# Kernel tuning notes

Hardware: AMD Instinct MI355X
Metric: run time of the kernel (lower is better)

The kernel has to match this reference:

```python
import jax, jax.numpy as jnp
import numpy as np

B, S, H = 4, 4096, 256

def setup_inputs() -> dict:
    key = jax.random.key(0)
    ks = jax.random.split(key, 7)
    s = 1.0 / np.sqrt(H)
    return {
        "x": jax.random.normal(ks[0], (B, S, H), dtype=jnp.float32),
        "Wq": jax.random.normal(ks[1], (H, H), dtype=jnp.float32) * s,
        "bq": jax.random.normal(ks[2], (H,), dtype=jnp.float32) * 0.01,
        "Wk": jax.random.normal(ks[3], (H, H), dtype=jnp.float32) * s,
        "bk": jax.random.normal(ks[4], (H,), dtype=jnp.float32) * 0.01,
        "Wv": jax.random.normal(ks[5], (H, H), dtype=jnp.float32) * s,
        "bv": jax.random.normal(ks[6], (H,), dtype=jnp.float32) * 0.01,
    }

def reference(x, Wq, bq, Wk, bk, Wv, bv):
    # Linear projections (torch Linear: x @ W^T + b; here W stored as [in,out])
    Q = jnp.einsum('bsh,hd->bsd', x, Wq) + bq
    K = jnp.einsum('bsh,hd->bsd', x, Wk) + bk
    V = jnp.einsum('bsh,hd->bsd', x, Wv) + bv
    scale = 1.0 / jnp.sqrt(jnp.float32(x.shape[-1]))
    scores = jnp.einsum('bqd,bkd->bqk', Q, K) * scale  # [B,S,S]
    weights = jax.nn.softmax(scores, axis=-1)
    return jnp.einsum('bqk,bkd->bqd', weights, V)
```

## Files before the change

### kernel.cpp

```cpp
#include <hip/hip_runtime.h>
#include <hip/hip_bf16.h>
#include <stdint.h>
#include <stddef.h>


typedef __bf16 bf16;
typedef _Float16 f16;
typedef __attribute__((ext_vector_type(4))) __bf16 bf16x4;
typedef __attribute__((ext_vector_type(8))) __bf16 bf16x8;
typedef __attribute__((ext_vector_type(4))) float f32x4;
typedef __attribute__((ext_vector_type(4))) _Float16 f16x4;
typedef __attribute__((ext_vector_type(8))) _Float16 f16x8;

#define S_LEN 4096
#define HDIM  256
#define PSTRIDE ((size_t)16384 * 256)

__device__ __forceinline__ f32x4 mfma16(bf16x8 a, bf16x8 b, f32x4 c) {
  return __builtin_amdgcn_mfma_f32_16x16x32_bf16(a, b, c, 0, 0, 0);
}

__device__ __forceinline__ void gld_lds16(const void* g, void* l) {
  __builtin_amdgcn_global_load_lds(
      (const __attribute__((address_space(1))) void*)g,
      (__attribute__((address_space(3))) void*)l, 16, 0, 0);
}

__device__ __forceinline__ float fast_exp2(float x) {
  float r;
  asm("v_exp_f32 %0, %1" : "=v"(r) : "v"(x));
  return r;
}

#define BAR_VMCNT4() do { \
  asm volatile("s_waitcnt vmcnt(4)" ::: "memory"); \
  __builtin_amdgcn_s_barrier(); \
  asm volatile("" ::: "memory"); \
  __builtin_amdgcn_sched_barrier(0); } while (0)
#define BAR_VMCNT0() do { \
  asm volatile("s_waitcnt vmcnt(0)" ::: "memory"); \
  __builtin_amdgcn_s_barrier(); \
  asm volatile("" ::: "memory"); \
  __builtin_amdgcn_sched_barrier(0); } while (0)

__global__ __launch_bounds__(256) void wt_kernel(
    const float* __restrict__ Wq, const float* __restrict__ Wk,
    const float* __restrict__ Wv, bf16* __restrict__ WT) {
  __shared__ float tile[32][33];
  int bid = blockIdx.x;
  int m = bid >> 6;
  int t = bid & 63;
  int hb = (t >> 3) * 32;
  int db = (t & 7) * 32;
  const float* W = (m == 0) ? Wq : (m == 1) ? Wk : Wv;
  bf16* o = WT + m * 65536;
  int ty = threadIdx.x >> 3;
  int tx = threadIdx.x & 7;
  float4 v = *(const float4*)(W + (size_t)(hb + ty) * 256 + db + tx * 4);
  tile[ty][tx * 4 + 0] = v.x; tile[ty][tx * 4 + 1] = v.y;
  tile[ty][tx * 4 + 2] = v.z; tile[ty][tx * 4 + 3] = v.w;
  __syncthreads();
  bf16x4 h = {(bf16)tile[tx * 4 + 0][ty], (bf16)tile[tx * 4 + 1][ty],
              (bf16)tile[tx * 4 + 2][ty], (bf16)tile[tx * 4 + 3][ty]};
  *(bf16x4*)(o + (size_t)(db + ty) * 256 + hb + tx * 4) = h;
}

__global__ __launch_bounds__(256, 3) void proj_kernel(
    const float* __restrict__ x, const bf16* __restrict__ WT,
    const float* __restrict__ bq, const float* __restrict__ bk,
    const float* __restrict__ bv,
    bf16* __restrict__ Qb, char* __restrict__ KV) {
  __shared__ __align__(16) char smem[34816];
  int tid = threadIdx.x;
  int row0 = blockIdx.x * 64;
  int m = blockIdx.y;

#pragma unroll
  for (int i = 0; i < 16; ++i) {
    int c = i * 256 + tid;
    int r = c >> 6, c4 = c & 63;
    float4 v = *(const float4*)(x + (size_t)(row0 + r) * 256 + c4 * 4);
    bf16x4 b4 = {(bf16)v.x, (bf16)v.y, (bf16)v.z, (bf16)v.w};
    *(bf16x4*)(smem + r * 512 + ((c4 * 8) ^ ((r & 7) << 4))) = b4;
  }
  __syncthreads();

  int w = tid >> 6, lane = tid & 63, lg = lane >> 4, l15 = lane & 15;
  int ar = w * 16 + l15;
  int swz = (l15 & 7) << 4;
  bf16x8 af[8];
#pragma unroll
  for (int ks = 0; ks < 8; ++ks)
    af[ks] = *(const bf16x8*)(smem + ar * 512 + ((ks * 64 + lg * 16) ^ swz));
  __syncthreads();

  int b = row0 >> 12, t0 = (row0 & 4095) >> 5;
  const bf16* Wm = WT + m * 65536;
  const float* bias = (m == 0) ? bq : (m == 1) ? bk : bv;

#pragma unroll
  for (int i = 0; i < 4; ++i) {
    int c = w * 4 + i;
    gld_lds16(Wm + (c * 16 + l15) * 256 + lg * 8, smem + c * 1024 + lane * 16);
  }
  __syncthreads();

  f32x4 acc[16];
#pragma unroll
  for (int dt = 0; dt < 16; ++dt) acc[dt] = f32x4{0.f, 0.f, 0.f, 0.f};

  for (int ks = 0; ks < 8; ++ks) {
    const char* wb = smem + (ks & 1) * 16384;
    if (ks + 1 < 8) {
      char* wn = smem + ((ks + 1) & 1) * 16384;
#pragma unroll
      for (int i = 0; i < 4; ++i) {
        int c = w * 4 + i;
        gld_lds16(Wm + (c * 16 + l15) * 256 + (ks + 1) * 32 + lg * 8,
                  wn + c * 1024 + lane * 16);
      }
    }
    __builtin_amdgcn_s_setprio(1);
#pragma unroll
    for (int dt = 0; dt < 16; ++dt) {
      bf16x8 wf = *(const bf16x8*)(wb + dt * 1024 + lane * 16);
      acc[dt] = mfma16(af[ks], wf, acc[dt]);
    }
    __builtin_amdgcn_s_setprio(0);
    __syncthreads();
  }

  if (m == 0) {
#pragma unroll
    for (int dt = 0; dt < 16; ++dt) {
      float bb = bias[dt * 16 + l15];
#pragma unroll
      for (int rr = 0; rr < 4; ++rr) {
        int srow = row0 + w * 16 + 4 * lg + rr;
        Qb[(size_t)srow * 256 + dt * 16 + l15] = (bf16)(acc[dt][rr] + bb);
      }
    }
  } else if (m == 1) {
    bf16* sm16 = (bf16*)smem;
#pragma unroll
    for (int dt = 0; dt < 16; ++dt) {
      float bb = bias[dt * 16 + l15];
#pragma unroll
      for (int rr = 0; rr < 4; ++rr) {
        int sl = w * 16 + 4 * lg + rr;
        sm16[sl * 264 + dt * 16 + l15] = (bf16)(acc[dt][rr] + bb);
      }
    }
    __syncthreads();
    int tt = tid >> 7, c = (tid >> 3) & 15, j0 = (tid & 7) * 8;
    char* dst = KV + ((size_t)(b * 128 + t0 + tt)) * 32768 + c * 1024 + j0 * 16;
#pragma unroll
    for (int u = 0; u < 8; ++u) {
      int l = j0 + u;
      bf16x8 v8 = *(const bf16x8*)(sm16 + (tt * 32 + (c & 1) * 16 + (l & 15)) * 264
                                   + (c >> 1) * 32 + (l >> 4) * 8);
      *(bf16x8*)(dst + u * 16) = v8;
    }
  } else {
    bf16* smV = (bf16*)smem;
#pragma unroll
    for (int dt = 0; dt < 16; ++dt) {
      float bb = bias[dt * 16 + l15];
      bf16x4 h = {(bf16)(acc[dt][0] + bb), (bf16)(acc[dt][1] + bb),
                  (bf16)(acc[dt][2] + bb), (bf16)(acc[dt][3] + bb)};
      *(bf16x4*)(smV + (dt * 16 + l15) * 68 + w * 16 + 4 * lg) = h;
    }
    __syncthreads();
    int tt = tid >> 7, c = (tid >> 3) & 15, j0 = (tid & 7) * 8;
    char* dst = KV + ((size_t)(b * 128 + t0 + tt)) * 32768 + 16384
                + c * 1024 + j0 * 16;
#pragma unroll
    for (int u = 0; u < 8; ++u) {
      int l = j0 + u;
      const bf16* p = smV + (c * 16 + (l & 15)) * 68 + tt * 32 + 4 * (l >> 4);
      bf16x4 lo = *(const bf16x4*)p;
      bf16x4 hi = *(const bf16x4*)(p + 16);
      bf16x8 v8 = __builtin_shufflevector(lo, hi, 0, 1, 2, 3, 4, 5, 6, 7);
      *(bf16x8*)(dst + u * 16) = v8;
    }
  }
}

__global__ __launch_bounds__(256, 2) void attn_kernel(
    const bf16* __restrict__ Qb, const char* __restrict__ KV,
    f16* __restrict__ P, float* __restrict__ ml, int nsplit, int ntiles) {
  __shared__ __align__(16) char smem[65536];

  int id = blockIdx.x;
  int b, sp, qb;
  if (nsplit == 4)      { int g = id & 15; b = g & 3;  sp = g >> 2; qb = id >> 4; }
  else if (nsplit == 2) { int g = id & 7;  b = g >> 1; sp = g & 1;  qb = id >> 3; }
  else                  { b = id & 3; sp = 0; qb = id >> 2; }

  int tid = threadIdx.x;
  int w = tid >> 6, lane = tid & 63, lg = lane >> 4, l15 = lane & 15;

  const char* kvsrc = KV + ((size_t)(b * 128 + sp * ntiles)) * 32768;

  int qrow0 = b * S_LEN + qb * 128 + w * 32 + l15;
  bf16x8 qf[2][8];
#pragma unroll
  for (int qs = 0; qs < 2; ++qs) {
    const bf16* Qr = Qb + (size_t)(qrow0 + qs * 16) * HDIM;
#pragma unroll
    for (int ks = 0; ks < 8; ++ks)
      qf[qs][ks] = *(const bf16x8*)(Qr + ks * 32 + lg * 8);
  }

  f32x4 acc[2][16];
#pragma unroll
  for (int qs = 0; qs < 2; ++qs)
#pragma unroll
    for (int dt = 0; dt < 16; ++dt) acc[qs][dt] = f32x4{0.f, 0.f, 0.f, 0.f};
  float lsum[2] = {0.f, 0.f};
  const float C = 0.09016844005556021f;

#pragma unroll
  for (int i = 0; i < 8; ++i)
    gld_lds16(kvsrc + i * 4096 + tid * 16, smem + i * 4096 + tid * 16);
  BAR_VMCNT0();

  for (int t = 0; t < ntiles; ++t) {
    int cur = (t & 1) << 15;
    const char* kb = smem + cur;
    const char* vb = kb + 16384;
    const char* s2 = kvsrc + (size_t)(t + 1) * 32768;
    char* d2 = smem + (cur ^ 32768);
    bool pre = (t + 1 < ntiles);

    if (pre) {
#pragma unroll
      for (int i = 0; i < 4; ++i)
        gld_lds16(s2 + i * 4096 + tid * 16, d2 + i * 4096 + tid * 16);
    }

    f32x4 st[2][2];
    st[0][0] = f32x4{0.f, 0.f, 0.f, 0.f}; st[0][1] = st[0][0];
    st[1][0] = st[0][0];                   st[1][1] = st[0][0];
    __builtin_amdgcn_s_setprio(1);
#pragma unroll
    for (int ks = 0; ks < 8; ++ks) {
      bf16x8 k0 = *(const bf16x8*)(kb + (ks * 2 + 0) * 1024 + lane * 16);
      bf16x8 k1 = *(const bf16x8*)(kb + (ks * 2 + 1) * 1024 + lane * 16);
      st[0][0] = mfma16(k0, qf[0][ks], st[0][0]);
      st[1][0] = mfma16(k0, qf[1][ks], st[1][0]);
      st[0][1] = mfma16(k1, qf[0][ks], st[0][1]);
      st[1][1] = mfma16(k1, qf[1][ks], st[1][1]);
    }
    __builtin_amdgcn_s_setprio(0);

    if (pre) BAR_VMCNT4(); else BAR_VMCNT0();

    if (pre) {
#pragma unroll
      for (int i = 4; i < 8; ++i)
        gld_lds16(s2 + i * 4096 + tid * 16, d2 + i * 4096 + tid * 16);
    }

    bf16x8 pf[2];
#pragma unroll
    for (int qs = 0; qs < 2; ++qs) {
      float ps = 0.f;
#pragma unroll
      for (int e = 0; e < 8; ++e) {
        float pv = fast_exp2(st[qs][e >> 2][e & 3] * C);
        ps += pv;
        pf[qs][e] = (bf16)pv;
      }
      lsum[qs] += ps;
    }

    __builtin_amdgcn_s_setprio(1);
#pragma unroll
    for (int dt = 0; dt < 16; ++dt) {
      bf16x8 vf = *(const bf16x8*)(vb + dt * 1024 + lane * 16);
      acc[0][dt] = mfma16(vf, pf[0], acc[0][dt]);
      acc[1][dt] = mfma16(vf, pf[1], acc[1][dt]);
    }
    __builtin_amdgcn_s_setprio(0);

    if (pre) BAR_VMCNT4();
  }

  f16* Pp = P + (size_t)sp * PSTRIDE;
#pragma unroll
  for (int qs = 0; qs < 2; ++qs) {
    float l = lsum[qs];
    l += __shfl_xor(l, 16, 64);
    l += __shfl_xor(l, 32, 64);
    int qrow = qrow0 + qs * 16;
    f16* prow = Pp + (size_t)qrow * HDIM;
#pragma unroll
    for (int dt = 0; dt < 16; ++dt) {
      f32x4 a = acc[qs][dt];
      f16x4 h = {(f16)a[0], (f16)a[1], (f16)a[2], (f16)a[3]};
      *(f16x4*)(prow + dt * 16 + 4 * lg) = h;
    }
    if (lane < 16) ml[sp * 16384 + qrow] = l;
  }
}

__global__ __launch_bounds__(256) void combine_kernel(
    float* __restrict__ out, const f16* __restrict__ P,
    const float* __restrict__ ml, int nsplit) {
  int chunk = blockIdx.x * 256 + threadIdx.x;
  int q = chunk >> 5;
  size_t base = (size_t)chunk * 8;

  float l = 0.f;
  float o[8] = {0.f, 0.f, 0.f, 0.f, 0.f, 0.f, 0.f, 0.f};
  for (int sp = 0; sp < nsplit; ++sp) {
    l += ml[sp * 16384 + q];
    f16x8 v = *(const f16x8*)(P + sp * PSTRIDE + base);
#pragma unroll
    for (int j = 0; j < 8; ++j) o[j] += (float)v[j];
  }
  float inv = 1.0f / l;
  f32x4 o0 = {o[0] * inv, o[1] * inv, o[2] * inv, o[3] * inv};
  f32x4 o1 = {o[4] * inv, o[5] * inv, o[6] * inv, o[7] * inv};
  *(f32x4*)(out + base) = o0;
  *(f32x4*)(out + base + 4) = o1;
}

extern "C" void kernel_launch(void* const* d_in, const int* in_sizes, int n_in,
                              void* d_out, int out_size, void* d_ws, size_t ws_size,
                              hipStream_t stream) {
  (void)in_sizes; (void)n_in; (void)out_size;
  const float* x  = (const float*)d_in[0];
  const float* Wq = (const float*)d_in[1];
  const float* bq = (const float*)d_in[2];
  const float* Wk = (const float*)d_in[3];
  const float* bk = (const float*)d_in[4];
  const float* Wv = (const float*)d_in[5];
  const float* bv = (const float*)d_in[6];

  char* ws = (char*)d_ws;
  bf16*  Qb = (bf16*)(ws);
  char*  KV = ws + (8u << 20);
  bf16*  WT = (bf16*)(ws + (24u << 20));
  float* ml = (float*)(ws + (24u << 20) + (512u << 10));
  f16*   P  = (f16*)(ws + (26u << 20));

  size_t need4 = ((size_t)26 << 20) + 4 * ((size_t)8 << 20);
  size_t need2 = ((size_t)26 << 20) + 2 * ((size_t)8 << 20);
  int nsplit = (ws_size >= need4) ? 4 : (ws_size >= need2) ? 2 : 1;
  int ntiles = (S_LEN / nsplit) / 32;
  int nblocks = 128 * nsplit;

  wt_kernel<<<192, 256, 0, stream>>>(Wq, Wk, Wv, WT);
  proj_kernel<<<dim3(256, 3), 256, 0, stream>>>(x, WT, bq, bk, bv, Qb, KV);
  attn_kernel<<<nblocks, 256, 0, stream>>>(Qb, KV, P, ml, nsplit, ntiles);
  combine_kernel<<<2048, 256, 0, stream>>>((float*)d_out, P, ml, nsplit);
}
```

Before: 109.5 us.

## Switch attention MFMAs from 16x16x32 to 32x32x16 with matching K/V layout

Replaces the 16x16x32 bf16 MFMA tiling in the attention kernel with 32x32x16 MFMAs. Each wave now owns 32 query rows as one tile, so QK^T takes 16 larger MFMAs per tile and PV takes 16 instead of 32 smaller ones. The projection kernel's K and V repacking into global memory is changed to match the 32-row operand layout. The goal is fewer MFMA issues and fewer LDS fragment reads per FLOP, at the cost of different register pressure and a different output write pattern.

```diff
diff --git a/kernel.cpp b/kernel.cpp
--- a/kernel.cpp
+++ b/kernel.cpp
@@ -9,6 +9,7 @@
 typedef __attribute__((ext_vector_type(4))) __bf16 bf16x4;
 typedef __attribute__((ext_vector_type(8))) __bf16 bf16x8;
 typedef __attribute__((ext_vector_type(4))) float f32x4;
+typedef __attribute__((ext_vector_type(16))) float f32x16;
 typedef __attribute__((ext_vector_type(4))) _Float16 f16x4;
 typedef __attribute__((ext_vector_type(8))) _Float16 f16x8;
 
@@ -18,6 +19,9 @@
 
 __device__ __forceinline__ f32x4 mfma16(bf16x8 a, bf16x8 b, f32x4 c) {
   return __builtin_amdgcn_mfma_f32_16x16x32_bf16(a, b, c, 0, 0, 0);
+}
+__device__ __forceinline__ f32x16 mfma32(bf16x8 a, bf16x8 b, f32x16 c) {
+  return __builtin_amdgcn_mfma_f32_32x32x16_bf16(a, b, c, 0, 0, 0);
 }
 
 __device__ __forceinline__ void gld_lds16(const void* g, void* l) {
@@ -157,8 +161,8 @@
 #pragma unroll
     for (int u = 0; u < 8; ++u) {
       int l = j0 + u;
-      bf16x8 v8 = *(const bf16x8*)(sm16 + (tt * 32 + (c & 1) * 16 + (l & 15)) * 264
-                                   + (c >> 1) * 32 + (l >> 4) * 8);
+      bf16x8 v8 = *(const bf16x8*)(sm16 + (tt * 32 + (l & 31)) * 264
+                                   + c * 16 + (l >> 5) * 8);
       *(bf16x8*)(dst + u * 16) = v8;
     }
   } else {
@@ -171,16 +175,18 @@
       *(bf16x4*)(smV + (dt * 16 + l15) * 68 + w * 16 + 4 * lg) = h;
     }
     __syncthreads();
-    int tt = tid >> 7, c = (tid >> 3) & 15, j0 = (tid & 7) * 8;
+    int tt = tid >> 7, c2 = (tid >> 3) & 15, j0 = (tid & 7) * 8;
+    int dt = c2 >> 1, ks = c2 & 1;
     char* dst = KV + ((size_t)(b * 128 + t0 + tt)) * 32768 + 16384
-                + c * 1024 + j0 * 16;
+                + c2 * 1024 + j0 * 16;
 #pragma unroll
     for (int u = 0; u < 8; ++u) {
       int l = j0 + u;
-      const bf16* p = smV + (c * 16 + (l & 15)) * 68 + tt * 32 + 4 * (l >> 4);
+      const bf16* p = smV + (dt * 32 + (l & 31)) * 68 + tt * 32
+                      + ks * 16 + 4 * (l >> 5);
       bf16x4 lo = *(const bf16x4*)p;
-      bf16x4 hi = *(const bf16x4*)(p + 16);
-      bf16x8 v8 = __builtin_shufflevector(lo, hi, 0, 1, 2, 3, 4, 5, 6, 7);
+      bf16x4 hi4 = *(const bf16x4*)(p + 8);
+      bf16x8 v8 = __builtin_shufflevector(lo, hi4, 0, 1, 2, 3, 4, 5, 6, 7);
       *(bf16x8*)(dst + u * 16) = v8;
     }
   }
@@ -198,26 +204,23 @@
   else                  { b = id & 3; sp = 0; qb = id >> 2; }
 
   int tid = threadIdx.x;
-  int w = tid >> 6, lane = tid & 63, lg = lane >> 4, l15 = lane & 15;
+  int w = tid >> 6, lane = tid & 63, hi = lane >> 5, l31 = lane & 31;
 
   const char* kvsrc = KV + ((size_t)(b * 128 + sp * ntiles)) * 32768;
 
-  int qrow0 = b * S_LEN + qb * 128 + w * 32 + l15;
-  bf16x8 qf[2][8];
-#pragma unroll
-  for (int qs = 0; qs < 2; ++qs) {
-    const bf16* Qr = Qb + (size_t)(qrow0 + qs * 16) * HDIM;
-#pragma unroll
-    for (int ks = 0; ks < 8; ++ks)
-      qf[qs][ks] = *(const bf16x8*)(Qr + ks * 32 + lg * 8);
-  }
-
-  f32x4 acc[2][16];
-#pragma unroll
-  for (int qs = 0; qs < 2; ++qs)
-#pragma unroll
-    for (int dt = 0; dt < 16; ++dt) acc[qs][dt] = f32x4{0.f, 0.f, 0.f, 0.f};
-  float lsum[2] = {0.f, 0.f};
+  int qrow = b * S_LEN + qb * 128 + w * 32 + l31;
+  const bf16* Qr = Qb + (size_t)qrow * HDIM;
+  bf16x8 qf[16];
+#pragma unroll
+  for (int c = 0; c < 16; ++c)
+    qf[c] = *(const bf16x8*)(Qr + c * 16 + hi * 8);
+
+  f32x16 acc[8];
+#pragma unroll
+  for (int dt = 0; dt < 8; ++dt)
+#pragma unroll
+    for (int r = 0; r < 16; ++r) acc[dt][r] = 0.f;
+  float lsum = 0.f;
   const float C = 0.09016844005556021f;
 
 #pragma unroll
@@ -239,18 +242,14 @@
         gld_lds16(s2 + i * 4096 + tid * 16, d2 + i * 4096 + tid * 16);
     }
 
-    f32x4 st[2][2];
-    st[0][0] = f32x4{0.f, 0.f, 0.f, 0.f}; st[0][1] = st[0][0];
-    st[1][0] = st[0][0];                   st[1][1] = st[0][0];
+    f32x16 st;
+#pragma unroll
+    for (int r = 0; r < 16; ++r) st[r] = 0.f;
     __builtin_amdgcn_s_setprio(1);
 #pragma unroll
-    for (int ks = 0; ks < 8; ++ks) {
-      bf16x8 k0 = *(const bf16x8*)(kb + (ks * 2 + 0) * 1024 + lane * 16);
-      bf16x8 k1 = *(const bf16x8*)(kb + (ks * 2 + 1) * 1024 + lane * 16);
-      st[0][0] = mfma16(k0, qf[0][ks], st[0][0]);
-      st[1][0] = mfma16(k0, qf[1][ks], st[1][0]);
-      st[0][1] = mfma16(k1, qf[0][ks], st[0][1]);
-      st[1][1] = mfma16(k1, qf[1][ks], st[1][1]);
+    for (int c = 0; c < 16; ++c) {
+      bf16x8 kf = *(const bf16x8*)(kb + c * 1024 + lane * 16);
+      st = mfma32(kf, qf[c], st);
     }
     __builtin_amdgcn_s_setprio(0);
 
@@ -262,47 +261,44 @@
         gld_lds16(s2 + i * 4096 + tid * 16, d2 + i * 4096 + tid * 16);
     }
 
+    float p[16];
+    float ps = 0.f;
+#pragma unroll
+    for (int r = 0; r < 16; ++r) {
+      p[r] = fast_exp2(st[r] * C);
+      ps += p[r];
+    }
+    lsum += ps;
     bf16x8 pf[2];
 #pragma unroll
-    for (int qs = 0; qs < 2; ++qs) {
-      float ps = 0.f;
-#pragma unroll
-      for (int e = 0; e < 8; ++e) {
-        float pv = fast_exp2(st[qs][e >> 2][e & 3] * C);
-        ps += pv;
-        pf[qs][e] = (bf16)pv;
+    for (int ks = 0; ks < 2; ++ks)
+#pragma unroll
+      for (int e = 0; e < 8; ++e) pf[ks][e] = (bf16)p[e + 8 * ks];
+
+    __builtin_amdgcn_s_setprio(1);
+#pragma unroll
+    for (int ks = 0; ks < 2; ++ks)
+#pragma unroll
+      for (int dt = 0; dt < 8; ++dt) {
+        bf16x8 vf = *(const bf16x8*)(vb + (dt * 2 + ks) * 1024 + lane * 16);
+        acc[dt] = mfma32(vf, pf[ks], acc[dt]);
       }
-      lsum[qs] += ps;
-    }
-
-    __builtin_amdgcn_s_setprio(1);
-#pragma unroll
-    for (int dt = 0; dt < 16; ++dt) {
-      bf16x8 vf = *(const bf16x8*)(vb + dt * 1024 + lane * 16);
-      acc[0][dt] = mfma16(vf, pf[0], acc[0][dt]);
-      acc[1][dt] = mfma16(vf, pf[1], acc[1][dt]);
-    }
     __builtin_amdgcn_s_setprio(0);
 
     if (pre) BAR_VMCNT4();
   }
 
-  f16* Pp = P + (size_t)sp * PSTRIDE;
-#pragma unroll
-  for (int qs = 0; qs < 2; ++qs) {
-    float l = lsum[qs];
-    l += __shfl_xor(l, 16, 64);
-    l += __shfl_xor(l, 32, 64);
-    int qrow = qrow0 + qs * 16;
-    f16* prow = Pp + (size_t)qrow * HDIM;
-#pragma unroll
-    for (int dt = 0; dt < 16; ++dt) {
-      f32x4 a = acc[qs][dt];
-      f16x4 h = {(f16)a[0], (f16)a[1], (f16)a[2], (f16)a[3]};
-      *(f16x4*)(prow + dt * 16 + 4 * lg) = h;
-    }
-    if (lane < 16) ml[sp * 16384 + qrow] = l;
-  }
+  lsum += __shfl_xor(lsum, 32, 64);
+  f16* prow = P + (size_t)sp * PSTRIDE + (size_t)qrow * HDIM;
+#pragma unroll
+  for (int dt = 0; dt < 8; ++dt)
+#pragma unroll
+    for (int rb = 0; rb < 4; ++rb) {
+      f16x4 h = {(f16)acc[dt][rb * 4 + 0], (f16)acc[dt][rb * 4 + 1],
+                 (f16)acc[dt][rb * 4 + 2], (f16)acc[dt][rb * 4 + 3]};
+      *(f16x4*)(prow + dt * 32 + rb * 8 + 4 * hi) = h;
+    }
+  if (lane < 32) ml[sp * 16384 + qrow] = lsum;
 }
 
 __global__ __launch_bounds__(256) void combine_kernel(
```

Measured after the change: 116.0 us. 1.06x slower.

## Halve attention query tile and use three-slot rotating LDS buffer

Applied to the files above, without the earlier changes.

Each attention block now handles 64 query rows instead of 128, one 16-row slice per wave, and the grid doubles. The double-buffered 64KB K/V staging becomes a 48KB three-slot rotation where the next K and next V are loaded into freed slots, so three blocks can fit per CU and register pressure drops. The cost is that every K/V tile is read from L2/HBM twice as often and each block does less MFMA work per LDS load, lowering data reuse.

```diff
diff --git a/kernel.cpp b/kernel.cpp
--- a/kernel.cpp
+++ b/kernel.cpp
@@ -186,10 +186,10 @@
   }
 }
 
-__global__ __launch_bounds__(256, 2) void attn_kernel(
+__global__ __launch_bounds__(256, 3) void attn_kernel(
     const bf16* __restrict__ Qb, const char* __restrict__ KV,
     f16* __restrict__ P, float* __restrict__ ml, int nsplit, int ntiles) {
-  __shared__ __align__(16) char smem[65536];
+  __shared__ __align__(16) char smem[49152];
 
   int id = blockIdx.x;
   int b, sp, qb;
@@ -202,55 +202,48 @@
 
   const char* kvsrc = KV + ((size_t)(b * 128 + sp * ntiles)) * 32768;
 
-  int qrow0 = b * S_LEN + qb * 128 + w * 32 + l15;
-  bf16x8 qf[2][8];
-#pragma unroll
-  for (int qs = 0; qs < 2; ++qs) {
-    const bf16* Qr = Qb + (size_t)(qrow0 + qs * 16) * HDIM;
-#pragma unroll
-    for (int ks = 0; ks < 8; ++ks)
-      qf[qs][ks] = *(const bf16x8*)(Qr + ks * 32 + lg * 8);
-  }
-
-  f32x4 acc[2][16];
-#pragma unroll
-  for (int qs = 0; qs < 2; ++qs)
-#pragma unroll
-    for (int dt = 0; dt < 16; ++dt) acc[qs][dt] = f32x4{0.f, 0.f, 0.f, 0.f};
-  float lsum[2] = {0.f, 0.f};
+  int qrow = b * S_LEN + qb * 64 + w * 16 + l15;
+  const bf16* Qr = Qb + (size_t)qrow * HDIM;
+  bf16x8 qf[8];
+#pragma unroll
+  for (int ks = 0; ks < 8; ++ks)
+    qf[ks] = *(const bf16x8*)(Qr + ks * 32 + lg * 8);
+
+  f32x4 acc[16];
+#pragma unroll
+  for (int dt = 0; dt < 16; ++dt) acc[dt] = f32x4{0.f, 0.f, 0.f, 0.f};
+  float lsum = 0.f;
   const float C = 0.09016844005556021f;
 
 #pragma unroll
-  for (int i = 0; i < 8; ++i)
+  for (int i = 0; i < 4; ++i)
     gld_lds16(kvsrc + i * 4096 + tid * 16, smem + i * 4096 + tid * 16);
+#pragma unroll
+  for (int i = 0; i < 4; ++i)
+    gld_lds16(kvsrc + 16384 + i * 4096 + tid * 16,
+              smem + 16384 + i * 4096 + tid * 16);
   BAR_VMCNT0();
 
+  int ks_s = 0, vs_s = 16384, fr_s = 32768;
   for (int t = 0; t < ntiles; ++t) {
-    int cur = (t & 1) << 15;
-    const char* kb = smem + cur;
-    const char* vb = kb + 16384;
+    bool pre = (t + 1 < ntiles);
     const char* s2 = kvsrc + (size_t)(t + 1) * 32768;
-    char* d2 = smem + (cur ^ 32768);
-    bool pre = (t + 1 < ntiles);
 
     if (pre) {
 #pragma unroll
       for (int i = 0; i < 4; ++i)
-        gld_lds16(s2 + i * 4096 + tid * 16, d2 + i * 4096 + tid * 16);
-    }
-
-    f32x4 st[2][2];
-    st[0][0] = f32x4{0.f, 0.f, 0.f, 0.f}; st[0][1] = st[0][0];
-    st[1][0] = st[0][0];                   st[1][1] = st[0][0];
+        gld_lds16(s2 + i * 4096 + tid * 16, smem + fr_s + i * 4096 + tid * 16);
+    }
+
+    const char* kb = smem + ks_s;
+    f32x4 st0 = {0.f, 0.f, 0.f, 0.f}, st1 = {0.f, 0.f, 0.f, 0.f};
     __builtin_amdgcn_s_setprio(1);
 #pragma unroll
     for (int ks = 0; ks < 8; ++ks) {
       bf16x8 k0 = *(const bf16x8*)(kb + (ks * 2 + 0) * 1024 + lane * 16);
       bf16x8 k1 = *(const bf16x8*)(kb + (ks * 2 + 1) * 1024 + lane * 16);
-      st[0][0] = mfma16(k0, qf[0][ks], st[0][0]);
-      st[1][0] = mfma16(k0, qf[1][ks], st[1][0]);
-      st[0][1] = mfma16(k1, qf[0][ks], st[0][1]);
-      st[1][1] = mfma16(k1, qf[1][ks], st[1][1]);
+      st0 = mfma16(k0, qf[ks], st0);
+      st1 = mfma16(k1, qf[ks], st1);
     }
     __builtin_amdgcn_s_setprio(0);
 
@@ -258,51 +251,49 @@
 
     if (pre) {
 #pragma unroll
-      for (int i = 4; i < 8; ++i)
-        gld_lds16(s2 + i * 4096 + tid * 16, d2 + i * 4096 + tid * 16);
-    }
-
-    bf16x8 pf[2];
-#pragma unroll
-    for (int qs = 0; qs < 2; ++qs) {
-      float ps = 0.f;
-#pragma unroll
-      for (int e = 0; e < 8; ++e) {
-        float pv = fast_exp2(st[qs][e >> 2][e & 3] * C);
-        ps += pv;
-        pf[qs][e] = (bf16)pv;
-      }
-      lsum[qs] += ps;
-    }
-
+      for (int i = 0; i < 4; ++i)
+        gld_lds16(s2 + 16384 + i * 4096 + tid * 16,
+                  smem + ks_s + i * 4096 + tid * 16);
+    }
+
+    bf16x8 pf;
+    float ps = 0.f;
+#pragma unroll
+    for (int e = 0; e < 8; ++e) {
+      float sv = (e < 4) ? st0[e & 3] : st1[e & 3];
+      float pv = fast_exp2(sv * C);
+      ps += pv;
+      pf[e] = (bf16)pv;
+    }
+    lsum += ps;
+
+    const char* vb = smem + vs_s;
     __builtin_amdgcn_s_setprio(1);
 #pragma unroll
     for (int dt = 0; dt < 16; ++dt) {
       bf16x8 vf = *(const bf16x8*)(vb + dt * 1024 + lane * 16);
-      acc[0][dt] = mfma16(vf, pf[0], acc[0][dt]);
-      acc[1][dt] = mfma16(vf, pf[1], acc[1][dt]);
+      acc[dt] = mfma16(vf, pf, acc[dt]);
     }
     __builtin_amdgcn_s_setprio(0);
 
     if (pre) BAR_VMCNT4();
-  }
-
-  f16* Pp = P + (size_t)sp * PSTRIDE;
-#pragma unroll
-  for (int qs = 0; qs < 2; ++qs) {
-    float l = lsum[qs];
-    l += __shfl_xor(l, 16, 64);
-    l += __shfl_xor(l, 32, 64);
-    int qrow = qrow0 + qs * 16;
-    f16* prow = Pp + (size_t)qrow * HDIM;
-#pragma unroll
-    for (int dt = 0; dt < 16; ++dt) {
-      f32x4 a = acc[qs][dt];
-      f16x4 h = {(f16)a[0], (f16)a[1], (f16)a[2], (f16)a[3]};
-      *(f16x4*)(prow + dt * 16 + 4 * lg) = h;
-    }
-    if (lane < 16) ml[sp * 16384 + qrow] = l;
-  }
+
+    int old_ks = ks_s;
+    ks_s = fr_s;
+    fr_s = vs_s;
+    vs_s = old_ks;
+  }
+
+  lsum += __shfl_xor(lsum, 16, 64);
+  lsum += __shfl_xor(lsum, 32, 64);
+  f16* prow = P + (size_t)sp * PSTRIDE + (size_t)qrow * HDIM;
+#pragma unroll
+  for (int dt = 0; dt < 16; ++dt) {
+    f32x4 a = acc[dt];
+    f16x4 h = {(f16)a[0], (f16)a[1], (f16)a[2], (f16)a[3]};
+    *(f16x4*)(prow + dt * 16 + 4 * lg) = h;
+  }
+  if (lane < 16) ml[sp * 16384 + qrow] = lsum;
 }
 
 __global__ __launch_bounds__(256) void combine_kernel(
@@ -350,7 +341,7 @@
   size_t need2 = ((size_t)26 << 20) + 2 * ((size_t)8 << 20);
   int nsplit = (ws_size >= need4) ? 4 : (ws_size >= need2) ? 2 : 1;
   int ntiles = (S_LEN / nsplit) / 32;
-  int nblocks = 128 * nsplit;
+  int nblocks = 256 * nsplit;
 
   wt_kernel<<<192, 256, 0, stream>>>(Wq, Wk, Wv, WT);
   proj_kernel<<<dim3(256, 3), 256, 0, stream>>>(x, WT, bq, bk, bv, Qb, KV);
```

Result: slower. 125.7 us (+14.8%).
